# Kernel optimization log

Hardware: AMD Instinct MI355X
Metric: run time of the kernel (lower is better)

Reference implementation:

```python
import jax, jax.numpy as jnp
import numpy as np

K0 = 0.7978845608028654  # sqrt(2/pi)
C1 = 0.044715

def _gelu_tanh(x):
    # tanh-approx GELU, matching the Triton kernel's math
    return 0.5 * x * (1.0 + jnp.tanh(K0 * (x + C1 * x * x * x)))

def setup_inputs() -> dict:
    key = jax.random.key(0)
    k1, k2, k3 = jax.random.split(key, 3)
    B, C_in, H, W = 32, 64, 128, 128
    C_out, KH = 128, 3
    x = jax.random.normal(k1, (B, C_in, H, W), dtype=jnp.float32)
    weight = jax.random.normal(k2, (C_out, C_in, KH, KH), dtype=jnp.float32)
    bias = jax.random.normal(k3, (C_out,), dtype=jnp.float32)
    return {"x": x, "weight": weight, "bias": bias}

def reference(x, weight, bias):
    # Valid conv2d, stride 1 (NCHW, OIHW)
    y = jax.lax.conv_general_dilated(
        x, weight,
        window_strides=(1, 1), padding="VALID",
        dimension_numbers=("NCHW", "OIHW", "NCHW"))
    y = y + bias[None, :, None, None]
    y = _gelu_tanh(y)
    # global average pool over spatial dims -> [B, C_out]
    return jnp.mean(y, axis=(2, 3))
```

## Files before the change

### kernel.cpp

```cpp
#include <hip/hip_runtime.h>
#include <cstdint>
#include <cstddef>

#define GK0 0.7978845608028654f
#define GC1 0.044715f

typedef __attribute__((ext_vector_type(8))) short short8;
typedef __attribute__((ext_vector_type(4))) float floatx4;

__device__ __forceinline__ unsigned short f2bf(float f) {
  union { float f; unsigned int u; } v; v.f = f;
  unsigned int r = v.u + 0x7fffu + ((v.u >> 16) & 1u);
  return (unsigned short)(r >> 16);
}

__device__ __forceinline__ void gl_lds16(const unsigned short* g, unsigned short* l) {
  __builtin_amdgcn_global_load_lds(
      (const __attribute__((address_space(1))) unsigned int*)g,
      (__attribute__((address_space(3))) unsigned int*)l, 16, 0, 0);
}

__global__ void k_wt(const float* __restrict__ w, unsigned short* __restrict__ wt,
                     float* __restrict__ out) {
  if (blockIdx.x == 0) {
    for (int i = threadIdx.x; i < 32 * 128; i += 256) out[i] = 0.0f;
  }
  int t = blockIdx.x * 256 + threadIdx.x;
  if (t >= 128 * 64 * 9) return;
  int co = t / 576; int r = t - co * 576; int ci = r / 9; int khw = r - ci * 9;
  wt[(khw * 128 + co) * 64 + ci] = f2bf(w[t]);
}

__global__ __launch_bounds__(256) void k_xt(const float* __restrict__ x,
                                            unsigned short* __restrict__ xb) {
  __shared__ float tile[64 * 132];
  const int tid = threadIdx.x, lane = tid & 63, wv = tid >> 6;
  const int b = blockIdx.y, h = blockIdx.x;
  const int w4 = lane & 31, cih = lane >> 5;

#pragma unroll
  for (int j = 0; j < 8; j++) {
    const int ci = wv * 16 + 2 * j + cih;
    float4 f = *(const float4*)(x + ((size_t)(b * 64 + ci) * 128 + h) * 128 + 4 * w4);
    *(float4*)((char*)tile + ci * 528 + ((16 * w4) ^ (((ci >> 3) & 7) << 4))) = f;
  }
  __syncthreads();
  unsigned short* orow = xb + ((size_t)b * 128 + h) * 8192;
  const int oct = tid & 7, wlo = tid >> 3;
#pragma unroll
  for (int it = 0; it < 4; it++) {
    const int w = wlo + 32 * it;
    short8 v;
#pragma unroll
    for (int j = 0; j < 8; j++) {
      const float f =
          *(const float*)((const char*)tile + (8 * oct + j) * 528 + ((4 * w) ^ (oct << 4)));
      v[j] = (short)f2bf(f);
    }
    *(short8*)(orow + w * 64 + oct * 8) = v;
  }
}

__global__ __launch_bounds__(256, 2) void k_conv(
    const unsigned short* __restrict__ xb, const unsigned short* __restrict__ wt,
    const float* __restrict__ bias, float* __restrict__ out) {
  __shared__ __align__(16) unsigned short Bs[2][9216];
  const int tid = threadIdx.x, lane = tid & 63, wv = tid >> 6;
  const int w0 = blockIdx.x * 64, h0 = blockIdx.y * 2, b = blockIdx.z;
  const int wm = wv & 1, wn = wv >> 1;
  const int m = lane & 15, q = lane >> 4;
  const int swz = ((lane >> 3) << 6) + (((lane & 7) ^ (lane >> 3)) << 3);

  floatx4 acc[4][4];
#pragma unroll
  for (int i = 0; i < 4; i++)
#pragma unroll
    for (int j = 0; j < 4; j++) acc[i][j] = (floatx4){0.f, 0.f, 0.f, 0.f};

  const unsigned short* xbb = xb + (size_t)b * 128 * 8192;

  auto stage = [&](unsigned short* bs, int row0) {
    for (int c = wv; c < 18; c += 4) {
      const int rh = (c >= 9) ? 1 : 0;
      const int j = c - 9 * rh;
      gl_lds16(xbb + ((size_t)((row0 + rh) * 128 + w0) << 6) + j * 512 + swz,
               bs + rh * 4608 + j * 512);
    }
  };

  stage(Bs[0], h0);
  __syncthreads();

#pragma unroll
  for (int kh = 0; kh < 3; kh++) {
    if (kh < 2) stage(Bs[(kh + 1) & 1], h0 + kh + 1);
    const unsigned short* bsr = Bs[kh & 1] + wn * 4608;
#pragma unroll
    for (int kw = 0; kw < 3; kw++) {
      const int khw = kh * 3 + kw;
      const int xr = ((m + kw) & 7) << 3;
#pragma unroll
      for (int half = 0; half < 2; half++) {
        const int colb = half * 32 + q * 8;
        short8 a[4], bf[4];
#pragma unroll
        for (int mt = 0; mt < 4; mt++)
          a[mt] = *(const short8*)(wt + khw * 8192 + (wm * 64 + mt * 16 + m) * 64 + colb);
#pragma unroll
        for (int nt = 0; nt < 4; nt++)
          bf[nt] = *(const short8*)(bsr + (nt * 16 + m + kw) * 64 + (colb ^ xr));
#pragma unroll
        for (int mt = 0; mt < 4; mt++)
#pragma unroll
          for (int nt = 0; nt < 4; nt++)
            acc[mt][nt] =
                __builtin_amdgcn_mfma_f32_16x16x32_bf16(a[mt], bf[nt], acc[mt][nt], 0, 0, 0);
      }
    }
    __syncthreads();
  }

  const float inv_area = 1.0f / (126.0f * 126.0f);
  float* orow = out + b * 128;
#pragma unroll
  for (int mt = 0; mt < 4; mt++)
#pragma unroll
    for (int r2 = 0; r2 < 4; r2++) {
      const int co = wm * 64 + mt * 16 + q * 4 + r2;
      const float bv = bias[co];
      float s = 0.f;
#pragma unroll
      for (int nt = 0; nt < 4; nt++) {
        float y = acc[mt][nt][r2] + bv;
        float u = GK0 * (y + GC1 * y * y * y);
        float e = __expf(-2.0f * u);
        float g = y * __builtin_amdgcn_rcpf(1.0f + e);
        if (w0 + nt * 16 + m < 126) s += g;
      }
#pragma unroll
      for (int d = 1; d < 16; d <<= 1) s += __shfl_xor(s, d, 64);
      if (m == 0) atomicAdd(&orow[co], s * inv_area);
    }
}

extern "C" void kernel_launch(void* const* d_in, const int* in_sizes, int n_in,
                              void* d_out, int out_size, void* d_ws, size_t ws_size,
                              hipStream_t stream) {
  const float* x    = (const float*)d_in[0];
  const float* w    = (const float*)d_in[1];
  const float* bias = (const float*)d_in[2];
  float* out = (float*)d_out;

  const size_t xb_elems = (size_t)32 * 128 * 8192;
  unsigned short* xbuf = (unsigned short*)d_ws;
  unsigned short* wbuf = xbuf + xb_elems + 2048;
  if (ws_size < xb_elems * 2 + 4096 + (size_t)9 * 128 * 64 * 2) return;

  k_wt<<<288, 256, 0, stream>>>(w, wbuf, out);
  k_xt<<<dim3(128, 32), 256, 0, stream>>>(x, xbuf);
  k_conv<<<dim3(2, 63, 32), 256, 0, stream>>>(xbuf, wbuf, bias, out);
}
```

Baseline: 427.9 us.

## Fuse fp32-to-bf16 input transpose into conv kernel and stage weights in LDS

Removes the separate k_xt pass that wrote a bf16 channel-last copy of x to workspace. Instead, each conv block loads the four fp32 input rows it needs directly, converts them to bf16 and writes them into a swizzled LDS tile. Weights are now staged per (kh,kw) tap into double-buffered LDS with async global-to-LDS loads, replacing direct global loads. The aim is to drop the intermediate write and read of the bf16 copy plus one launch. In exchange, overlapping rows are read redundantly in fp32, the LDS stores are scalar 16-bit, LDS use grows, and there are now nine barriers instead of three.

Measured after the change: 400.7 us. -6.3%, faster.

```diff
diff --git a/kernel.cpp b/kernel.cpp
--- a/kernel.cpp
+++ b/kernel.cpp
@@ -31,45 +31,15 @@
   wt[(khw * 128 + co) * 64 + ci] = f2bf(w[t]);
 }
 
-__global__ __launch_bounds__(256) void k_xt(const float* __restrict__ x,
-                                            unsigned short* __restrict__ xb) {
-  __shared__ float tile[64 * 132];
-  const int tid = threadIdx.x, lane = tid & 63, wv = tid >> 6;
-  const int b = blockIdx.y, h = blockIdx.x;
-  const int w4 = lane & 31, cih = lane >> 5;
-
-#pragma unroll
-  for (int j = 0; j < 8; j++) {
-    const int ci = wv * 16 + 2 * j + cih;
-    float4 f = *(const float4*)(x + ((size_t)(b * 64 + ci) * 128 + h) * 128 + 4 * w4);
-    *(float4*)((char*)tile + ci * 528 + ((16 * w4) ^ (((ci >> 3) & 7) << 4))) = f;
-  }
-  __syncthreads();
-  unsigned short* orow = xb + ((size_t)b * 128 + h) * 8192;
-  const int oct = tid & 7, wlo = tid >> 3;
-#pragma unroll
-  for (int it = 0; it < 4; it++) {
-    const int w = wlo + 32 * it;
-    short8 v;
-#pragma unroll
-    for (int j = 0; j < 8; j++) {
-      const float f =
-          *(const float*)((const char*)tile + (8 * oct + j) * 528 + ((4 * w) ^ (oct << 4)));
-      v[j] = (short)f2bf(f);
-    }
-    *(short8*)(orow + w * 64 + oct * 8) = v;
-  }
-}
-
 __global__ __launch_bounds__(256, 2) void k_conv(
-    const unsigned short* __restrict__ xb, const unsigned short* __restrict__ wt,
+    const float* __restrict__ x, const unsigned short* __restrict__ wt,
     const float* __restrict__ bias, float* __restrict__ out) {
-  __shared__ __align__(16) unsigned short Bs[2][9216];
+  __shared__ __align__(16) unsigned short Bs[4 * 72 * 64];
+  __shared__ __align__(16) unsigned short As[2][8192];
   const int tid = threadIdx.x, lane = tid & 63, wv = tid >> 6;
   const int w0 = blockIdx.x * 64, h0 = blockIdx.y * 2, b = blockIdx.z;
   const int wm = wv & 1, wn = wv >> 1;
   const int m = lane & 15, q = lane >> 4;
-  const int swz = ((lane >> 3) << 6) + (((lane & 7) ^ (lane >> 3)) << 3);
 
   floatx4 acc[4][4];
 #pragma unroll
@@ -77,48 +47,63 @@
 #pragma unroll
     for (int j = 0; j < 4; j++) acc[i][j] = (floatx4){0.f, 0.f, 0.f, 0.f};
 
-  const unsigned short* xbb = xb + (size_t)b * 128 * 8192;
+  for (int r = 0; r < 4; r++) {
+    const float* xrow = x + ((size_t)(b * 64) * 128 + (h0 + r)) * 128;
+    unsigned short* brow = Bs + r * 4608;
+    for (int c = tid; c < 1152; c += 256) {
+      const int ci = c / 18, i = c - ci * 18;
+      const int wc = min(w0 + 4 * i, 124);
+      union { float4 v; float f[4]; } u;
+      u.v = *(const float4*)(xrow + (size_t)ci * 16384 + wc);
+#pragma unroll
+      for (int k2 = 0; k2 < 4; k2++) {
+        const int p = 4 * i + k2;
+        brow[p * 64 + (ci ^ ((p & 7) << 3))] = f2bf(u.f[k2]);
+      }
+    }
+  }
 
-  auto stage = [&](unsigned short* bs, int row0) {
-    for (int c = wv; c < 18; c += 4) {
-      const int rh = (c >= 9) ? 1 : 0;
-      const int j = c - 9 * rh;
-      gl_lds16(xbb + ((size_t)((row0 + rh) * 128 + w0) << 6) + j * 512 + swz,
-               bs + rh * 4608 + j * 512);
+  auto stageA = [&](unsigned short* dst, int khw) {
+    const unsigned short* src = wt + khw * 8192;
+#pragma unroll
+    for (int i = 0; i < 4; i++) {
+      const int chunk = wv * 4 + i;
+      gl_lds16(src + chunk * 512 + (lane >> 3) * 64 + (((lane & 7) ^ (lane >> 3)) << 3),
+               dst + chunk * 512);
     }
   };
 
-  stage(Bs[0], h0);
+  stageA(As[0], 0);
   __syncthreads();
 
 #pragma unroll
-  for (int kh = 0; kh < 3; kh++) {
-    if (kh < 2) stage(Bs[(kh + 1) & 1], h0 + kh + 1);
-    const unsigned short* bsr = Bs[kh & 1] + wn * 4608;
+  for (int kh = 0; kh < 3; kh++)
 #pragma unroll
     for (int kw = 0; kw < 3; kw++) {
       const int khw = kh * 3 + kw;
-      const int xr = ((m + kw) & 7) << 3;
+      if (khw < 8) stageA(As[(khw + 1) & 1], khw + 1);
+      const unsigned short* acur = As[khw & 1] + wm * 4096;
+      const unsigned short* bcur = Bs + (wn + kh) * 4608;
 #pragma unroll
       for (int half = 0; half < 2; half++) {
         const int colb = half * 32 + q * 8;
         short8 a[4], bf[4];
 #pragma unroll
         for (int mt = 0; mt < 4; mt++)
-          a[mt] = *(const short8*)(wt + khw * 8192 + (wm * 64 + mt * 16 + m) * 64 + colb);
+          a[mt] = *(const short8*)(acur + (mt * 16 + m) * 64 + (colb ^ ((m & 7) << 3)));
 #pragma unroll
         for (int nt = 0; nt < 4; nt++)
-          bf[nt] = *(const short8*)(bsr + (nt * 16 + m + kw) * 64 + (colb ^ xr));
+          bf[nt] = *(const short8*)(bcur + (nt * 16 + m + kw) * 64 +
+                                    (colb ^ (((m + kw) & 7) << 3)));
 #pragma unroll
         for (int mt = 0; mt < 4; mt++)
 #pragma unroll
           for (int nt = 0; nt < 4; nt++)
-            acc[mt][nt] =
-                __builtin_amdgcn_mfma_f32_16x16x32_bf16(a[mt], bf[nt], acc[mt][nt], 0, 0, 0);
+            acc[mt][nt] = __builtin_amdgcn_mfma_f32_16x16x32_bf16(
+                a[mt], bf[nt], acc[mt][nt], 0, 0, 0);
       }
+      __syncthreads();
     }
-    __syncthreads();
-  }
 
   const float inv_area = 1.0f / (126.0f * 126.0f);
   float* orow = out + b * 128;
@@ -151,12 +136,9 @@
   const float* bias = (const float*)d_in[2];
   float* out = (float*)d_out;
 
-  const size_t xb_elems = (size_t)32 * 128 * 8192;
-  unsigned short* xbuf = (unsigned short*)d_ws;
-  unsigned short* wbuf = xbuf + xb_elems + 2048;
-  if (ws_size < xb_elems * 2 + 4096 + (size_t)9 * 128 * 64 * 2) return;
+  unsigned short* wbuf = (unsigned short*)d_ws;
+  if (ws_size < (size_t)9 * 128 * 64 * 2 + 4096) return;
 
   k_wt<<<288, 256, 0, stream>>>(w, wbuf, out);
-  k_xt<<<dim3(128, 32), 256, 0, stream>>>(x, xbuf);
-  k_conv<<<dim3(2, 63, 32), 256, 0, stream>>>(xbuf, wbuf, bias, out);
+  k_conv<<<dim3(2, 63, 32), 256, 0, stream>>>(x, wbuf, bias, out);
 }
```
